# Performance work log

Measured on AMD Instinct MI355X. Metric: run time of the kernel, lower is better.

## Reference

```python
import jax, jax.numpy as jnp
import numpy as np

EPS_BN = 1e-5
NEG_SLOPE = 0.2

def _bn(x, gamma, beta):
    # BatchNorm1d using batch statistics (training-mode math, biased var as torch)
    mu = jnp.mean(x, axis=0)
    var = jnp.var(x, axis=0)
    return (x - mu) * jax.lax.rsqrt(var + EPS_BN) * gamma + beta

def _gat(x, src, dst, W, att_src, att_dst, bias, N):
    # x: [N, Fin]; W: [Fin, H*C]; att_*: [H, C]
    H, C = att_src.shape
    h = (x @ W).reshape(N, H, C)                       # [N,H,C]
    a_src = jnp.sum(h * att_src, axis=-1)              # [N,H]
    a_dst = jnp.sum(h * att_dst, axis=-1)              # [N,H]
    alpha = jax.nn.leaky_relu(a_src[src] + a_dst[dst], NEG_SLOPE)  # [E,H]
    # segment softmax over destination nodes
    m = jax.ops.segment_max(alpha, dst, num_segments=N)           # [N,H]
    e = jnp.exp(alpha - m[dst])
    s = jax.ops.segment_sum(e, dst, num_segments=N)
    a = e / (s[dst] + 1e-16)                           # [E,H]
    msg = h[src] * a[:, :, None]                       # [E,H,C]
    out = jax.ops.segment_sum(msg, dst, num_segments=N)  # [N,H,C]
    return out.reshape(N, H * C) + bias

def setup_inputs() -> dict:
    key = jax.random.key(0)
    ks = jax.random.split(key, 16)
    N, Fin, Hid = 50000, 128, 64
    E = 800000
    x = jax.random.normal(ks[0], (N, Fin), dtype=jnp.float32)
    edge_index = jax.random.randint(ks[1], (2, E), 0, N, dtype=jnp.int32)
    sc = 0.1
    return {
        'x': x,
        'edge_index': edge_index,
        'W1': jax.random.normal(ks[2], (Fin, 2 * Hid), jnp.float32) * sc,
        'att_src1': jax.random.normal(ks[3], (2, Hid), jnp.float32) * sc,
        'att_dst1': jax.random.normal(ks[4], (2, Hid), jnp.float32) * sc,
        'b1': jnp.zeros((2 * Hid,), jnp.float32),
        'g1': jnp.ones((2 * Hid,), jnp.float32),
        'be1': jnp.zeros((2 * Hid,), jnp.float32),
        'W2': jax.random.normal(ks[5], (2 * Hid, Hid), jnp.float32) * sc,
        'att_src2': jax.random.normal(ks[6], (1, Hid), jnp.float32) * sc,
        'att_dst2': jax.random.normal(ks[7], (1, Hid), jnp.float32) * sc,
        'b2': jnp.zeros((Hid,), jnp.float32),
        'g2': jnp.ones((Hid,), jnp.float32),
        'be2': jnp.zeros((Hid,), jnp.float32),
        'linW': jax.random.normal(ks[8], (Hid, 1), jnp.float32) * sc,
        'linb': jnp.zeros((1,), jnp.float32),
    }

def reference(x, edge_index, W1, att_src1, att_dst1, b1, g1, be1,
              W2, att_src2, att_dst2, b2, g2, be2, linW, linb):
    N = x.shape[0]
    loops = jnp.arange(N, dtype=edge_index.dtype)
    src = jnp.concatenate([edge_index[0], loops])  # PyG adds self-loops
    dst = jnp.concatenate([edge_index[1], loops])
    h = _gat(x, src, dst, W1, att_src1, att_dst1, b1, N)
    h = jax.nn.relu(_bn(h, g1, be1))                 # dropout = identity (eval)
    h = _gat(h, src, dst, W2, att_src2, att_dst2, b2, N)
    h = jax.nn.relu(_bn(h, g2, be2))
    return (h @ linW + linb).squeeze(-1)
```

## Files before the change

kernel.cpp:

```cpp
#include <hip/hip_runtime.h>
#include <hip/hip_fp16.h>
#include <math.h>

#define LEAKY 0.2f
#define XPAD 136
#define MAXB 512

typedef _Float16 f16x8 __attribute__((ext_vector_type(8)));
typedef float f32x4 __attribute__((ext_vector_type(4)));

__device__ inline int h2i(__half2 h) { union { __half2 h; int i; } u; u.h = h; return u.i; }
__device__ inline __half2 i2h(int i) { union { __half2 h; int i; } u; u.i = i; return u.h; }


__global__ __launch_bounds__(256) void k_bhist(const int* __restrict__ ei,
                                               int* __restrict__ gbcnt, int E, int PB)
{
  __shared__ int lh[MAXB];
  int t = threadIdx.x;
  for (int i = t; i < PB; i += 256) lh[i] = 0;
  __syncthreads();
  int base = blockIdx.x * 2048;
#pragma unroll
  for (int k = 0; k < 8; ++k) {
    int idx = base + t + k * 256;
    if (idx < E) atomicAdd(&lh[ei[E + idx] >> 7], 1);
  }
  __syncthreads();
  for (int i = t; i < PB; i += 256) if (lh[i]) atomicAdd(&gbcnt[i], lh[i]);
}

__global__ __launch_bounds__(512) void k_bscan(const int* __restrict__ gbcnt,
                                               int* __restrict__ pbase,
                                               int* __restrict__ gcur, int PB)
{
  __shared__ int ls[512];
  int t = threadIdx.x;
  int v = (t < PB) ? gbcnt[t] : 0;
  ls[t] = v;
  __syncthreads();
  for (int off = 1; off < 512; off <<= 1) {
    int u = (t >= off) ? ls[t - off] : 0;
    __syncthreads();
    ls[t] += u;
    __syncthreads();
  }
  int excl = ls[t] - v;
  if (t <= PB) pbase[t] = excl;
  if (t < PB) gcur[t] = excl;
}

__global__ __launch_bounds__(256) void k_part(const int* __restrict__ ei,
                                              int* __restrict__ gcur,
                                              int2* __restrict__ pairs, int E, int PB)
{
  __shared__ int lcnt[MAXB], lbase[MAXB];
  int t = threadIdx.x;
  for (int i = t; i < PB; i += 256) lcnt[i] = 0;
  __syncthreads();
  int base = blockIdx.x * 4096;
  int lp[16];
#pragma unroll
  for (int k = 0; k < 16; ++k) {
    int idx = base + t + k * 256;
    int pk = -1;
    if (idx < E) {
      int b = ei[E + idx] >> 7;
      int p = atomicAdd(&lcnt[b], 1);
      pk = (p << 10) | b;
    }
    lp[k] = pk;
  }
  __syncthreads();
  for (int b = t; b < PB; b += 256) lbase[b] = atomicAdd(&gcur[b], lcnt[b]);
  __syncthreads();
#pragma unroll
  for (int k = 0; k < 16; ++k) {
    if (lp[k] >= 0) {
      int idx = base + t + k * 256;
      int b = lp[k] & 1023, p = lp[k] >> 10;
      pairs[lbase[b] + p] = make_int2(ei[idx], ei[E + idx]);
    }
  }
}

__global__ __launch_bounds__(256) void k_fine(const int2* __restrict__ pairs,
                                              const int* __restrict__ pbase,
                                              int* __restrict__ rowptr,
                                              int* __restrict__ colx, int N)
{
  __shared__ int ldeg[128], lcur[128];
  int b = blockIdx.x, t = threadIdx.x;
  int nbase = b << 7;
  int nbn = N - nbase; if (nbn > 128) nbn = 128;
  if (t < 128) ldeg[t] = (t < nbn) ? 1 : 0;
  __syncthreads();
  int e0 = pbase[b], e1 = pbase[b + 1];
  for (int e = e0 + t; e < e1; e += 256) atomicAdd(&ldeg[pairs[e].y - nbase], 1);
  __syncthreads();
  int myv = (t < 128) ? ldeg[t] : 0;
  for (int off = 1; off < 128; off <<= 1) {
    int u = (t < 128 && t >= off) ? ldeg[t - off] : 0;
    __syncthreads();
    if (t < 128) ldeg[t] += u;
    __syncthreads();
  }
  int colx0 = e0 + nbase;
  if (t < 128) {
    int excl = ldeg[t] - myv;
    lcur[t] = colx0 + excl;
    int idx = nbase + t;
    if (idx <= N) rowptr[idx] = colx0 + excl;
  }
  __syncthreads();
  for (int e = e0 + t; e < e1; e += 256) {
    int2 p = pairs[e];
    int pos = atomicAdd(&lcur[p.y - nbase], 1);
    colx[pos] = p.x;
  }
  if (t < nbn) {
    int pos = atomicAdd(&lcur[t], 1);
    colx[pos] = nbase + t;
  }
}

__global__ __launch_bounds__(256) void k_gemm1(
    const float* __restrict__ x, const float* __restrict__ W,
    const float* __restrict__ att_s, const float* __restrict__ att_d,
    unsigned* __restrict__ h1h, float* __restrict__ a1s, float* __restrict__ a1d, int N)
{
  __shared__ __align__(16) _Float16 Xh[64 * XPAD];
  __shared__ __align__(16) _Float16 Wt[128 * XPAD];
  int t = threadIdx.x;
  const float4* W4 = (const float4*)W;
#pragma unroll
  for (int i = 0; i < 16; ++i) {
    int id = t + i * 256;
    int row = id >> 5, c0 = (id & 31) * 4;
    float4 wv = W4[id];
    Wt[(c0    ) * XPAD + row] = (_Float16)wv.x;
    Wt[(c0 + 1) * XPAD + row] = (_Float16)wv.y;
    Wt[(c0 + 2) * XPAD + row] = (_Float16)wv.z;
    Wt[(c0 + 3) * XPAD + row] = (_Float16)wv.w;
  }
  int row0 = blockIdx.x * 64;
  const float4* X4 = (const float4*)x;
#pragma unroll
  for (int i = 0; i < 8; ++i) {
    int id = t + i * 256;
    int r = id >> 5, c = id & 31;
    int gr = row0 + r;
    float4 v = (gr < N) ? X4[(size_t)gr * 32 + c] : make_float4(0.f, 0.f, 0.f, 0.f);
    unsigned p01 = (unsigned)h2i(__floats2half2_rn(v.x, v.y));
    unsigned p23 = (unsigned)h2i(__floats2half2_rn(v.z, v.w));
    *(uint2*)&Xh[r * XPAD + c * 4] = make_uint2(p01, p23);
  }
  __syncthreads();
  int w = t >> 6, l = t & 63;
  int m = l & 15, kg = l >> 4;
  f32x4 acc[8];
#pragma unroll
  for (int c = 0; c < 8; ++c) { acc[c][0] = 0.f; acc[c][1] = 0.f; acc[c][2] = 0.f; acc[c][3] = 0.f; }
#pragma unroll
  for (int ks = 0; ks < 4; ++ks) {
    f16x8 a = *(const f16x8*)&Xh[(w * 16 + m) * XPAD + ks * 32 + kg * 8];
#pragma unroll
    for (int c = 0; c < 8; ++c) {
      f16x8 bfr = *(const f16x8*)&Wt[(c * 16 + m) * XPAD + ks * 32 + kg * 8];
      acc[c] = __builtin_amdgcn_mfma_f32_16x16x32_f16(a, bfr, acc[c], 0, 0, 0);
    }
  }
#pragma unroll
  for (int c = 0; c < 8; ++c)
#pragma unroll
    for (int r = 0; r < 4; ++r)
      Xh[(w * 16 + kg * 4 + r) * XPAD + c * 16 + m] = (_Float16)acc[c][r];
  __syncthreads();
#pragma unroll
  for (int i = 0; i < 8; ++i) {
    int id = t + i * 256;
    int r = id >> 5, c4 = id & 31;
    int gr = row0 + r;
    uint2 pk = *(const uint2*)&Xh[r * XPAD + c4 * 4];
    float2 v01 = __half22float2(i2h((int)pk.x));
    float2 v23 = __half22float2(i2h((int)pk.y));
    int col = c4 * 4;
    float4 asv = *(const float4*)&att_s[col];
    float4 adv = *(const float4*)&att_d[col];
    float ps = v01.x * asv.x + v01.y * asv.y + v23.x * asv.z + v23.y * asv.w;
    float pd = v01.x * adv.x + v01.y * adv.y + v23.x * adv.z + v23.y * adv.w;
    ps += __shfl_xor(ps, 1); ps += __shfl_xor(ps, 2); ps += __shfl_xor(ps, 4); ps += __shfl_xor(ps, 8);
    pd += __shfl_xor(pd, 1); pd += __shfl_xor(pd, 2); pd += __shfl_xor(pd, 4); pd += __shfl_xor(pd, 8);
    if (gr < N) {
      *(uint2*)&h1h[(size_t)gr * 64 + c4 * 2] = pk;
      if ((t & 15) == 0) { int h = (t >> 4) & 1; a1s[gr * 2 + h] = ps; a1d[gr * 2 + h] = pd; }
    }
  }
}

__global__ __launch_bounds__(256) void k_agg1(
    const int* __restrict__ rowptr, const int* __restrict__ colx,
    const unsigned* __restrict__ h1h, const float* __restrict__ a1s,
    const float* __restrict__ a1d, const float* __restrict__ b1,
    unsigned* __restrict__ v1h, float* __restrict__ stats, int N)
{
  int t = threadIdx.x;
  int w = t >> 6, lane = t & 63;
  int g = lane >> 5, q = lane & 31;
  bool hi = q >= 16;
  int n = blockIdx.x * 8 + w * 2 + g;
  bool act = n < N;
  float4 bias = *(const float4*)&b1[q * 4];
  int start = 0, end = 0;
  float2 ad = make_float2(0.f, 0.f);
  if (act) { start = rowptr[n]; end = rowptr[n + 1]; ad = *(const float2*)&a1d[n * 2]; }
  float se = 0.f;
  float4 acc = {0, 0, 0, 0};
  for (int base = start; base < end; base += 32) {
    int cnt = end - base; if (cnt > 32) cnt = 32;
    int sl = 0, epk = 0;
    if (q < cnt) {
      sl = colx[base + q];
      float2 av = *(const float2*)&a1s[sl * 2];
      float x0 = av.x + ad.x, x1 = av.y + ad.y;
      x0 = (x0 > 0.f) ? x0 : LEAKY * x0;
      x1 = (x1 > 0.f) ? x1 : LEAKY * x1;
      epk = h2i(__floats2half2_rn(__expf(x0), __expf(x1)));
    }
    int j = 0;
    int lim16 = cnt & ~15;
    for (; j < lim16; j += 16) {
      int ss[16], ee[16];
#pragma unroll
      for (int k = 0; k < 16; ++k) { ss[k] = __shfl(sl, j + k, 32); ee[k] = __shfl(epk, j + k, 32); }
      uint2 rr[16];
#pragma unroll
      for (int k = 0; k < 16; ++k) rr[k] = *(const uint2*)&h1h[(size_t)ss[k] * 64 + q * 2];
#pragma unroll
      for (int k = 0; k < 16; ++k) {
        float2 ef = __half22float2(i2h(ee[k]));
        float wg = hi ? ef.y : ef.x;
        float2 r01 = __half22float2(i2h((int)rr[k].x));
        float2 r23 = __half22float2(i2h((int)rr[k].y));
        se += wg;
        acc.x = fmaf(wg, r01.x, acc.x);
        acc.y = fmaf(wg, r01.y, acc.y);
        acc.z = fmaf(wg, r23.x, acc.z);
        acc.w = fmaf(wg, r23.y, acc.w);
      }
    }
    int lim8 = cnt & ~7;
    for (; j < lim8; j += 8) {
      int ss[8], ee[8];
#pragma unroll
      for (int k = 0; k < 8; ++k) { ss[k] = __shfl(sl, j + k, 32); ee[k] = __shfl(epk, j + k, 32); }
      uint2 rr[8];
#pragma unroll
      for (int k = 0; k < 8; ++k) rr[k] = *(const uint2*)&h1h[(size_t)ss[k] * 64 + q * 2];
#pragma unroll
      for (int k = 0; k < 8; ++k) {
        float2 ef = __half22float2(i2h(ee[k]));
        float wg = hi ? ef.y : ef.x;
        float2 r01 = __half22float2(i2h((int)rr[k].x));
        float2 r23 = __half22float2(i2h((int)rr[k].y));
        se += wg;
        acc.x = fmaf(wg, r01.x, acc.x);
        acc.y = fmaf(wg, r01.y, acc.y);
        acc.z = fmaf(wg, r23.x, acc.z);
        acc.w = fmaf(wg, r23.y, acc.w);
      }
    }
    for (; j < cnt; ++j) {
      int s0 = __shfl(sl, j, 32), e0 = __shfl(epk, j, 32);
      float2 ef = __half22float2(i2h(e0));
      float wg = hi ? ef.y : ef.x;
      uint2 rv = *(const uint2*)&h1h[(size_t)s0 * 64 + q * 2];
      float2 r01 = __half22float2(i2h((int)rv.x));
      float2 r23 = __half22float2(i2h((int)rv.y));
      se += wg;
      acc.x = fmaf(wg, r01.x, acc.x);
      acc.y = fmaf(wg, r01.y, acc.y);
      acc.z = fmaf(wg, r23.x, acc.z);
      acc.w = fmaf(wg, r23.y, acc.w);
    }
  }
  float4 o = {0, 0, 0, 0};
  if (act) {
    float inv = 1.f / se;
    o.x = fmaf(acc.x, inv, bias.x);
    o.y = fmaf(acc.y, inv, bias.y);
    o.z = fmaf(acc.z, inv, bias.z);
    o.w = fmaf(acc.w, inv, bias.w);
    unsigned p01 = (unsigned)h2i(__floats2half2_rn(o.x, o.y));
    unsigned p23 = (unsigned)h2i(__floats2half2_rn(o.z, o.w));
    *(uint2*)&v1h[(size_t)n * 64 + q * 2] = make_uint2(p01, p23);
  }
  __shared__ float4 reds[4][64], redq[4][64];
  reds[w][lane] = o;
  redq[w][lane] = make_float4(o.x * o.x, o.y * o.y, o.z * o.z, o.w * o.w);
  __syncthreads();
  if (t < 128) {
    int qq = t >> 2, ii = t & 3;
    float s = 0.f, sq = 0.f;
#pragma unroll
    for (int w2 = 0; w2 < 4; ++w2) {
      s  += (&reds[w2][qq].x)[ii] + (&reds[w2][qq + 32].x)[ii];
      sq += (&redq[w2][qq].x)[ii] + (&redq[w2][qq + 32].x)[ii];
    }
    int sl8 = (blockIdx.x & 7) * 256;
    atomicAdd(&stats[sl8 + t], s);
    atomicAdd(&stats[sl8 + 128 + t], sq);
  }
}

__global__ __launch_bounds__(256) void k_gemm2(
    const unsigned* __restrict__ v1h, const float* __restrict__ W2,
    const float* __restrict__ stats, const float* __restrict__ g1, const float* __restrict__ be1,
    const float* __restrict__ att_s, const float* __restrict__ att_d,
    unsigned* __restrict__ h2h, float* __restrict__ a2s, float* __restrict__ a2d,
    int N, float rcpN)
{
  __shared__ __align__(16) _Float16 Xh[64 * XPAD];
  __shared__ __align__(16) _Float16 Wt[64 * XPAD];
  __shared__ float kc[128], sc[128];
  int t = threadIdx.x;
  if (t < 128) {
    float su = 0.f, sq = 0.f;
#pragma unroll
    for (int s8 = 0; s8 < 8; ++s8) { su += stats[s8 * 256 + t]; sq += stats[s8 * 256 + 128 + t]; }
    float mu = su * rcpN;
    float var = sq * rcpN - mu * mu;
    float kk = g1[t] * rsqrtf(var + 1e-5f);
    kc[t] = kk; sc[t] = be1[t] - mu * kk;
  }
  const float4* W4 = (const float4*)W2;
#pragma unroll
  for (int i = 0; i < 8; ++i) {
    int id = t + i * 256;
    int row = id >> 4, c0 = (id & 15) * 4;
    float4 wv = W4[id];
    Wt[(c0    ) * XPAD + row] = (_Float16)wv.x;
    Wt[(c0 + 1) * XPAD + row] = (_Float16)wv.y;
    Wt[(c0 + 2) * XPAD + row] = (_Float16)wv.z;
    Wt[(c0 + 3) * XPAD + row] = (_Float16)wv.w;
  }
  __syncthreads();
  int row0 = blockIdx.x * 64;
#pragma unroll
  for (int i = 0; i < 8; ++i) {
    int id = t + i * 256;
    int r = id >> 5, c4 = id & 31;
    int gr = row0 + r;
    uint2 pv = (gr < N) ? *(const uint2*)&v1h[(size_t)gr * 64 + c4 * 2] : make_uint2(0, 0);
    float2 a01 = __half22float2(i2h((int)pv.x));
    float2 a23 = __half22float2(i2h((int)pv.y));
    int f0 = c4 * 4;
    float o0 = fmaxf(a01.x * kc[f0]     + sc[f0],     0.f);
    float o1 = fmaxf(a01.y * kc[f0 + 1] + sc[f0 + 1], 0.f);
    float o2 = fmaxf(a23.x * kc[f0 + 2] + sc[f0 + 2], 0.f);
    float o3 = fmaxf(a23.y * kc[f0 + 3] + sc[f0 + 3], 0.f);
    unsigned p01 = (unsigned)h2i(__floats2half2_rn(o0, o1));
    unsigned p23 = (unsigned)h2i(__floats2half2_rn(o2, o3));
    *(uint2*)&Xh[r * XPAD + c4 * 4] = make_uint2(p01, p23);
  }
  __syncthreads();
  int w = t >> 6, l = t & 63;
  int m = l & 15, kg = l >> 4;
  f32x4 acc[4];
#pragma unroll
  for (int c = 0; c < 4; ++c) { acc[c][0] = 0.f; acc[c][1] = 0.f; acc[c][2] = 0.f; acc[c][3] = 0.f; }
#pragma unroll
  for (int ks = 0; ks < 4; ++ks) {
    f16x8 a = *(const f16x8*)&Xh[(w * 16 + m) * XPAD + ks * 32 + kg * 8];
#pragma unroll
    for (int c = 0; c < 4; ++c) {
      f16x8 bfr = *(const f16x8*)&Wt[(c * 16 + m) * XPAD + ks * 32 + kg * 8];
      acc[c] = __builtin_amdgcn_mfma_f32_16x16x32_f16(a, bfr, acc[c], 0, 0, 0);
    }
  }
#pragma unroll
  for (int c = 0; c < 4; ++c)
#pragma unroll
    for (int r = 0; r < 4; ++r)
      Xh[(w * 16 + kg * 4 + r) * XPAD + c * 16 + m] = (_Float16)acc[c][r];
  __syncthreads();
#pragma unroll
  for (int i = 0; i < 4; ++i) {
    int id = t + i * 256;
    int r = id >> 4, c4 = id & 15;
    int gr = row0 + r;
    uint2 pk = *(const uint2*)&Xh[r * XPAD + c4 * 4];
    float2 v01 = __half22float2(i2h((int)pk.x));
    float2 v23 = __half22float2(i2h((int)pk.y));
    int col = c4 * 4;
    float4 asv = *(const float4*)&att_s[col];
    float4 adv = *(const float4*)&att_d[col];
    float ps = v01.x * asv.x + v01.y * asv.y + v23.x * asv.z + v23.y * asv.w;
    float pd = v01.x * adv.x + v01.y * adv.y + v23.x * adv.z + v23.y * adv.w;
    ps += __shfl_xor(ps, 1); ps += __shfl_xor(ps, 2); ps += __shfl_xor(ps, 4); ps += __shfl_xor(ps, 8);
    pd += __shfl_xor(pd, 1); pd += __shfl_xor(pd, 2); pd += __shfl_xor(pd, 4); pd += __shfl_xor(pd, 8);
    if (gr < N) {
      *(uint2*)&h2h[(size_t)gr * 32 + c4 * 2] = pk;
      if ((t & 15) == 0) { a2s[gr] = ps; a2d[gr] = pd; }
    }
  }
}

__global__ __launch_bounds__(256) void k_agg2(
    const int* __restrict__ rowptr, const int* __restrict__ colx,
    const unsigned* __restrict__ h2h, const float* __restrict__ a2s,
    const float* __restrict__ a2d, const float* __restrict__ b2,
    unsigned* __restrict__ v2h, float* __restrict__ stats, int N)
{
  int t = threadIdx.x;
  int w = t >> 6, lane = t & 63;
  int g = lane >> 4, q = lane & 15;
  int n = blockIdx.x * 16 + w * 4 + g;
  bool act = n < N;
  float4 bias = *(const float4*)&b2[q * 4];
  int start = 0, end = 0;
  float ad = 0.f;
  if (act) { start = rowptr[n]; end = rowptr[n + 1]; ad = a2d[n]; }
  float se = 0.f;
  float4 acc = {0, 0, 0, 0};
  for (int base = start; base < end; base += 16) {
    int cnt = end - base; if (cnt > 16) cnt = 16;
    int sl = 0; float ev = 0.f;
    if (q < cnt) {
      sl = colx[base + q];
      float av = a2s[sl] + ad;
      av = (av > 0.f) ? av : LEAKY * av;
      ev = __expf(av);
    }
    int j = 0;
    if (cnt == 16) {
      int ss[16]; float ee[16];
#pragma unroll
      for (int k = 0; k < 16; ++k) { ss[k] = __shfl(sl, k, 16); ee[k] = __shfl(ev, k, 16); }
      uint2 rr[16];
#pragma unroll
      for (int k = 0; k < 16; ++k) rr[k] = *(const uint2*)&h2h[(size_t)ss[k] * 32 + q * 2];
#pragma unroll
      for (int k = 0; k < 16; ++k) {
        float2 r01 = __half22float2(i2h((int)rr[k].x));
        float2 r23 = __half22float2(i2h((int)rr[k].y));
        se += ee[k];
        acc.x = fmaf(ee[k], r01.x, acc.x);
        acc.y = fmaf(ee[k], r01.y, acc.y);
        acc.z = fmaf(ee[k], r23.x, acc.z);
        acc.w = fmaf(ee[k], r23.y, acc.w);
      }
      j = 16;
    }
    int lim8 = cnt & ~7;
    for (; j < lim8; j += 8) {
      int ss[8]; float ee[8];
#pragma unroll
      for (int k = 0; k < 8; ++k) { ss[k] = __shfl(sl, j + k, 16); ee[k] = __shfl(ev, j + k, 16); }
      uint2 rr[8];
#pragma unroll
      for (int k = 0; k < 8; ++k) rr[k] = *(const uint2*)&h2h[(size_t)ss[k] * 32 + q * 2];
#pragma unroll
      for (int k = 0; k < 8; ++k) {
        float2 r01 = __half22float2(i2h((int)rr[k].x));
        float2 r23 = __half22float2(i2h((int)rr[k].y));
        se += ee[k];
        acc.x = fmaf(ee[k], r01.x, acc.x);
        acc.y = fmaf(ee[k], r01.y, acc.y);
        acc.z = fmaf(ee[k], r23.x, acc.z);
        acc.w = fmaf(ee[k], r23.y, acc.w);
      }
    }
    for (; j < cnt; ++j) {
      int s0 = __shfl(sl, j, 16);
      float e0 = __shfl(ev, j, 16);
      uint2 rv = *(const uint2*)&h2h[(size_t)s0 * 32 + q * 2];
      float2 r01 = __half22float2(i2h((int)rv.x));
      float2 r23 = __half22float2(i2h((int)rv.y));
      se += e0;
      acc.x = fmaf(e0, r01.x, acc.x);
      acc.y = fmaf(e0, r01.y, acc.y);
      acc.z = fmaf(e0, r23.x, acc.z);
      acc.w = fmaf(e0, r23.y, acc.w);
    }
  }
  float4 o = {0, 0, 0, 0};
  if (act) {
    float inv = 1.f / se;
    o.x = fmaf(acc.x, inv, bias.x);
    o.y = fmaf(acc.y, inv, bias.y);
    o.z = fmaf(acc.z, inv, bias.z);
    o.w = fmaf(acc.w, inv, bias.w);
    unsigned p01 = (unsigned)h2i(__floats2half2_rn(o.x, o.y));
    unsigned p23 = (unsigned)h2i(__floats2half2_rn(o.z, o.w));
    *(uint2*)&v2h[(size_t)n * 32 + q * 2] = make_uint2(p01, p23);
  }
  __shared__ float4 reds[4][64], redq[4][64];
  reds[w][lane] = o;
  redq[w][lane] = make_float4(o.x * o.x, o.y * o.y, o.z * o.z, o.w * o.w);
  __syncthreads();
  if (t < 64) {
    int qq = t >> 2, ii = t & 3;
    float s = 0.f, sq = 0.f;
#pragma unroll
    for (int w2 = 0; w2 < 4; ++w2) {
#pragma unroll
      for (int g2 = 0; g2 < 4; ++g2) {
        s  += (&reds[w2][g2 * 16 + qq].x)[ii];
        sq += (&redq[w2][g2 * 16 + qq].x)[ii];
      }
    }
    int sl8 = (blockIdx.x & 7) * 128;
    atomicAdd(&stats[sl8 + t], s);
    atomicAdd(&stats[sl8 + 64 + t], sq);
  }
}

__global__ __launch_bounds__(256) void k_out(
    const unsigned* __restrict__ v2h, const float* __restrict__ stats,
    const float* __restrict__ g2, const float* __restrict__ be2,
    const float* __restrict__ linW, const float* __restrict__ linb,
    float* __restrict__ out, int N, float rcpN)
{
  __shared__ float kc[64], sc[64], lw[64];
  int t = threadIdx.x;
  if (t < 64) {
    float su = 0.f, sq = 0.f;
#pragma unroll
    for (int s8 = 0; s8 < 8; ++s8) { su += stats[s8 * 128 + t]; sq += stats[s8 * 128 + 64 + t]; }
    float mu = su * rcpN;
    float var = sq * rcpN - mu * mu;
    float kk = g2[t] * rsqrtf(var + 1e-5f);
    kc[t] = kk; sc[t] = be2[t] - mu * kk; lw[t] = linW[t];
  }
  __syncthreads();
  int w = t >> 6, lane = t & 63, g = lane >> 5, q = lane & 31;
  int n = blockIdx.x * 8 + w * 2 + g;
  if (n >= N) return;
  unsigned uv = v2h[(size_t)n * 32 + q];
  float2 vf = __half22float2(i2h((int)uv));
  float h0 = fmaxf(vf.x * kc[2 * q] + sc[2 * q], 0.f);
  float h1 = fmaxf(vf.y * kc[2 * q + 1] + sc[2 * q + 1], 0.f);
  float p = fmaf(h0, lw[2 * q], h1 * lw[2 * q + 1]);
#pragma unroll
  for (int off = 16; off; off >>= 1) p += __shfl_xor(p, off, 32);
  if (q == 0) out[n] = p + linb[0];
}

extern "C" void kernel_launch(void* const* d_in, const int* in_sizes, int n_in,
                              void* d_out, int out_size, void* d_ws, size_t ws_size,
                              hipStream_t stream)
{
  const float* x    = (const float*)d_in[0];
  const int*   ei   = (const int*)d_in[1];
  const float* W1   = (const float*)d_in[2];
  const float* as1  = (const float*)d_in[3];
  const float* ad1  = (const float*)d_in[4];
  const float* b1   = (const float*)d_in[5];
  const float* g1   = (const float*)d_in[6];
  const float* be1  = (const float*)d_in[7];
  const float* W2   = (const float*)d_in[8];
  const float* as2  = (const float*)d_in[9];
  const float* ad2  = (const float*)d_in[10];
  const float* b2   = (const float*)d_in[11];
  const float* g2   = (const float*)d_in[12];
  const float* be2  = (const float*)d_in[13];
  const float* linW = (const float*)d_in[14];
  const float* linb = (const float*)d_in[15];
  float* out = (float*)d_out;

  int N = in_sizes[0] / 128;
  int E = in_sizes[1] / 2;
  int Etot = E + N;
  float rcpN = 1.f / (float)N;
  int PB = (N + 127) / 128;

  float* ws = (float*)d_ws;
  size_t o = 0;
  float* H1HF = ws + o; o += (size_t)N * 64;
  float* V1HF = ws + o; o += (size_t)N * 64;
  float* A1S  = ws + o; o += (size_t)N * 2;
  float* A1D  = ws + o; o += (size_t)N * 2;
  float* A2S  = ws + o; o += N;
  float* A2D  = ws + o; o += N;
  float* ST1  = ws + o; o += 8 * 256;
  float* ST2  = ws + o; o += 8 * 128;
  int* GBCNT  = (int*)(ws + o); o += MAXB;
  int* PBASE  = (int*)(ws + o); o += MAXB + 1;
  int* GCUR   = (int*)(ws + o); o += MAXB;
  int* ROWPTR = (int*)(ws + o); o += (size_t)N + 1;
  int* COL    = (int*)(ws + o); o += (size_t)Etot;
  int2* PAIRS = (int2*)(ws + o); o += (size_t)E * 2;
  unsigned* H1H = (unsigned*)H1HF;
  unsigned* H2H = (unsigned*)H1HF;
  unsigned* V1H = (unsigned*)V1HF;
  unsigned* V2H = (unsigned*)V1HF;

  hipMemsetAsync(ST1, 0, (3072 + MAXB) * 4, stream);

  int gb  = (N + 63) / 64;
  int bh  = (E + 2047) / 2048;
  int pt  = (E + 4095) / 4096;
  int ab1 = (N + 7) / 8;
  int ab2 = (N + 15) / 16;
  int ob  = (N + 7) / 8;

  k_bhist<<<bh, 256, 0, stream>>>(ei, GBCNT, E, PB);
  k_bscan<<<1, 512, 0, stream>>>(GBCNT, PBASE, GCUR, PB);
  k_part<<<pt, 256, 0, stream>>>(ei, GCUR, PAIRS, E, PB);
  k_fine<<<PB, 256, 0, stream>>>(PAIRS, PBASE, ROWPTR, COL, N);
  k_gemm1<<<gb, 256, 0, stream>>>(x, W1, as1, ad1, H1H, A1S, A1D, N);
  k_agg1<<<ab1, 256, 0, stream>>>(ROWPTR, COL, H1H, A1S, A1D, b1, V1H, ST1, N);
  k_gemm2<<<gb, 256, 0, stream>>>(V1H, W2, ST1, g1, be1, as2, ad2, H2H, A2S, A2D, N, rcpN);
  k_agg2<<<ab2, 256, 0, stream>>>(ROWPTR, COL, H2H, A2S, A2D, b2, V2H, ST2, N);
  k_out<<<ob, 256, 0, stream>>>(V2H, ST2, g2, be2, linW, linb, out, N, rcpN);
}
```

Baseline: 170.8 us.

## Widen agg1 gathers to 16-byte loads and split BatchNorm stats into separate kernels

The layer-1 aggregation kernel now assigns 16 lanes per destination node instead of 32. Each lane gathers a 16-byte chunk of the fp16 source row, which doubles the nodes per block and halves the shuffle and index overhead per edge. The BatchNorm sum and sum-of-squares reductions are moved out of both aggregation kernels into a templated k_stats kernel that rereads the fp16 outputs, which simplifies the aggregation epilogue but adds two launches and an extra pass over the activations. The statistics are now computed from fp16-rounded values rather than fp32 ones. k_part also keeps the src and dst indices in registers instead of reloading them from global memory for the scatter.

Result: slower. 179.5 us (+5.1%).

```diff
diff --git a/kernel.cpp b/kernel.cpp
--- a/kernel.cpp
+++ b/kernel.cpp
@@ -11,7 +11,6 @@
 
 __device__ inline int h2i(__half2 h) { union { __half2 h; int i; } u; u.h = h; return u.i; }
 __device__ inline __half2 i2h(int i) { union { __half2 h; int i; } u; u.i = i; return u.h; }
-
 
 __global__ __launch_bounds__(256) void k_bhist(const int* __restrict__ ei,
                                                int* __restrict__ gbcnt, int E, int PB)
@@ -59,17 +58,18 @@
   for (int i = t; i < PB; i += 256) lcnt[i] = 0;
   __syncthreads();
   int base = blockIdx.x * 4096;
-  int lp[16];
+  int lsrc[16], ldst[16], lp[16];
 #pragma unroll
   for (int k = 0; k < 16; ++k) {
     int idx = base + t + k * 256;
-    int pk = -1;
+    lp[k] = -1;
     if (idx < E) {
-      int b = ei[E + idx] >> 7;
+      int s = ei[idx], d = ei[E + idx];
+      lsrc[k] = s; ldst[k] = d;
+      int b = d >> 7;
       int p = atomicAdd(&lcnt[b], 1);
-      pk = (p << 10) | b;
-    }
-    lp[k] = pk;
+      lp[k] = (p << 10) | b;
+    }
   }
   __syncthreads();
   for (int b = t; b < PB; b += 256) lbase[b] = atomicAdd(&gcur[b], lcnt[b]);
@@ -77,9 +77,8 @@
 #pragma unroll
   for (int k = 0; k < 16; ++k) {
     if (lp[k] >= 0) {
-      int idx = base + t + k * 256;
       int b = lp[k] & 1023, p = lp[k] >> 10;
-      pairs[lbase[b] + p] = make_int2(ei[idx], ei[E + idx]);
+      pairs[lbase[b] + p] = make_int2(lsrc[k], ldst[k]);
     }
   }
 }
@@ -202,22 +201,23 @@
     const int* __restrict__ rowptr, const int* __restrict__ colx,
     const unsigned* __restrict__ h1h, const float* __restrict__ a1s,
     const float* __restrict__ a1d, const float* __restrict__ b1,
-    unsigned* __restrict__ v1h, float* __restrict__ stats, int N)
+    unsigned* __restrict__ v1h, int N)
 {
   int t = threadIdx.x;
   int w = t >> 6, lane = t & 63;
-  int g = lane >> 5, q = lane & 31;
-  bool hi = q >= 16;
-  int n = blockIdx.x * 8 + w * 2 + g;
+  int g = lane >> 4, q = lane & 15;
+  bool hi = q >= 8;
+  int n = blockIdx.x * 16 + w * 4 + g;
   bool act = n < N;
-  float4 bias = *(const float4*)&b1[q * 4];
+  float4 biasA = *(const float4*)&b1[q * 8];
+  float4 biasB = *(const float4*)&b1[q * 8 + 4];
   int start = 0, end = 0;
   float2 ad = make_float2(0.f, 0.f);
   if (act) { start = rowptr[n]; end = rowptr[n + 1]; ad = *(const float2*)&a1d[n * 2]; }
   float se = 0.f;
-  float4 acc = {0, 0, 0, 0};
-  for (int base = start; base < end; base += 32) {
-    int cnt = end - base; if (cnt > 32) cnt = 32;
+  float4 accA = {0, 0, 0, 0}, accB = {0, 0, 0, 0};
+  for (int base = start; base < end; base += 16) {
+    int cnt = end - base; if (cnt > 16) cnt = 16;
     int sl = 0, epk = 0;
     if (q < cnt) {
       sl = colx[base + q];
@@ -228,88 +228,115 @@
       epk = h2i(__floats2half2_rn(__expf(x0), __expf(x1)));
     }
     int j = 0;
-    int lim16 = cnt & ~15;
-    for (; j < lim16; j += 16) {
+    if (cnt == 16) {
       int ss[16], ee[16];
 #pragma unroll
-      for (int k = 0; k < 16; ++k) { ss[k] = __shfl(sl, j + k, 32); ee[k] = __shfl(epk, j + k, 32); }
-      uint2 rr[16];
-#pragma unroll
-      for (int k = 0; k < 16; ++k) rr[k] = *(const uint2*)&h1h[(size_t)ss[k] * 64 + q * 2];
+      for (int k = 0; k < 16; ++k) { ss[k] = __shfl(sl, k, 16); ee[k] = __shfl(epk, k, 16); }
+      uint4 rr[16];
+#pragma unroll
+      for (int k = 0; k < 16; ++k) rr[k] = *(const uint4*)&h1h[(size_t)ss[k] * 64 + q * 4];
 #pragma unroll
       for (int k = 0; k < 16; ++k) {
         float2 ef = __half22float2(i2h(ee[k]));
         float wg = hi ? ef.y : ef.x;
-        float2 r01 = __half22float2(i2h((int)rr[k].x));
-        float2 r23 = __half22float2(i2h((int)rr[k].y));
+        float2 r0 = __half22float2(i2h((int)rr[k].x));
+        float2 r1 = __half22float2(i2h((int)rr[k].y));
+        float2 r2 = __half22float2(i2h((int)rr[k].z));
+        float2 r3 = __half22float2(i2h((int)rr[k].w));
         se += wg;
-        acc.x = fmaf(wg, r01.x, acc.x);
-        acc.y = fmaf(wg, r01.y, acc.y);
-        acc.z = fmaf(wg, r23.x, acc.z);
-        acc.w = fmaf(wg, r23.y, acc.w);
+        accA.x = fmaf(wg, r0.x, accA.x); accA.y = fmaf(wg, r0.y, accA.y);
+        accA.z = fmaf(wg, r1.x, accA.z); accA.w = fmaf(wg, r1.y, accA.w);
+        accB.x = fmaf(wg, r2.x, accB.x); accB.y = fmaf(wg, r2.y, accB.y);
+        accB.z = fmaf(wg, r3.x, accB.z); accB.w = fmaf(wg, r3.y, accB.w);
       }
+      j = 16;
     }
     int lim8 = cnt & ~7;
     for (; j < lim8; j += 8) {
       int ss[8], ee[8];
 #pragma unroll
-      for (int k = 0; k < 8; ++k) { ss[k] = __shfl(sl, j + k, 32); ee[k] = __shfl(epk, j + k, 32); }
-      uint2 rr[8];
-#pragma unroll
-      for (int k = 0; k < 8; ++k) rr[k] = *(const uint2*)&h1h[(size_t)ss[k] * 64 + q * 2];
+      for (int k = 0; k < 8; ++k) { ss[k] = __shfl(sl, j + k, 16); ee[k] = __shfl(epk, j + k, 16); }
+      uint4 rr[8];
+#pragma unroll
+      for (int k = 0; k < 8; ++k) rr[k] = *(const uint4*)&h1h[(size_t)ss[k] * 64 + q * 4];
 #pragma unroll
       for (int k = 0; k < 8; ++k) {
         float2 ef = __half22float2(i2h(ee[k]));
         float wg = hi ? ef.y : ef.x;
-        float2 r01 = __half22float2(i2h((int)rr[k].x));
-        float2 r23 = __half22float2(i2h((int)rr[k].y));
+        float2 r0 = __half22float2(i2h((int)rr[k].x));
+        float2 r1 = __half22float2(i2h((int)rr[k].y));
+        float2 r2 = __half22float2(i2h((int)rr[k].z));
+        float2 r3 = __half22float2(i2h((int)rr[k].w));
         se += wg;
-        acc.x = fmaf(wg, r01.x, acc.x);
-        acc.y = fmaf(wg, r01.y, acc.y);
-        acc.z = fmaf(wg, r23.x, acc.z);
-        acc.w = fmaf(wg, r23.y, acc.w);
+        accA.x = fmaf(wg, r0.x, accA.x); accA.y = fmaf(wg, r0.y, accA.y);
+        accA.z = fmaf(wg, r1.x, accA.z); accA.w = fmaf(wg, r1.y, accA.w);
+        accB.x = fmaf(wg, r2.x, accB.x); accB.y = fmaf(wg, r2.y, accB.y);
+        accB.z = fmaf(wg, r3.x, accB.z); accB.w = fmaf(wg, r3.y, accB.w);
       }
     }
     for (; j < cnt; ++j) {
-      int s0 = __shfl(sl, j, 32), e0 = __shfl(epk, j, 32);
+      int s0 = __shfl(sl, j, 16), e0 = __shfl(epk, j, 16);
       float2 ef = __half22float2(i2h(e0));
       float wg = hi ? ef.y : ef.x;
-      uint2 rv = *(const uint2*)&h1h[(size_t)s0 * 64 + q * 2];
-      float2 r01 = __half22float2(i2h((int)rv.x));
-      float2 r23 = __half22float2(i2h((int)rv.y));
+      uint4 rv = *(const uint4*)&h1h[(size_t)s0 * 64 + q * 4];
+      float2 r0 = __half22float2(i2h((int)rv.x));
+      float2 r1 = __half22float2(i2h((int)rv.y));
+      float2 r2 = __half22float2(i2h((int)rv.z));
+      float2 r3 = __half22float2(i2h((int)rv.w));
       se += wg;
-      acc.x = fmaf(wg, r01.x, acc.x);
-      acc.y = fmaf(wg, r01.y, acc.y);
-      acc.z = fmaf(wg, r23.x, acc.z);
-      acc.w = fmaf(wg, r23.y, acc.w);
-    }
-  }
-  float4 o = {0, 0, 0, 0};
+      accA.x = fmaf(wg, r0.x, accA.x); accA.y = fmaf(wg, r0.y, accA.y);
+      accA.z = fmaf(wg, r1.x, accA.z); accA.w = fmaf(wg, r1.y, accA.w);
+      accB.x = fmaf(wg, r2.x, accB.x); accB.y = fmaf(wg, r2.y, accB.y);
+      accB.z = fmaf(wg, r3.x, accB.z); accB.w = fmaf(wg, r3.y, accB.w);
+    }
+  }
   if (act) {
     float inv = 1.f / se;
-    o.x = fmaf(acc.x, inv, bias.x);
-    o.y = fmaf(acc.y, inv, bias.y);
-    o.z = fmaf(acc.z, inv, bias.z);
-    o.w = fmaf(acc.w, inv, bias.w);
-    unsigned p01 = (unsigned)h2i(__floats2half2_rn(o.x, o.y));
-    unsigned p23 = (unsigned)h2i(__floats2half2_rn(o.z, o.w));
-    *(uint2*)&v1h[(size_t)n * 64 + q * 2] = make_uint2(p01, p23);
-  }
-  __shared__ float4 reds[4][64], redq[4][64];
-  reds[w][lane] = o;
-  redq[w][lane] = make_float4(o.x * o.x, o.y * o.y, o.z * o.z, o.w * o.w);
-  __syncthreads();
-  if (t < 128) {
-    int qq = t >> 2, ii = t & 3;
-    float s = 0.f, sq = 0.f;
-#pragma unroll
-    for (int w2 = 0; w2 < 4; ++w2) {
-      s  += (&reds[w2][qq].x)[ii] + (&reds[w2][qq + 32].x)[ii];
-      sq += (&redq[w2][qq].x)[ii] + (&redq[w2][qq + 32].x)[ii];
-    }
-    int sl8 = (blockIdx.x & 7) * 256;
-    atomicAdd(&stats[sl8 + t], s);
-    atomicAdd(&stats[sl8 + 128 + t], sq);
+    float4 oA, oB;
+    oA.x = fmaf(accA.x, inv, biasA.x);
+    oA.y = fmaf(accA.y, inv, biasA.y);
+    oA.z = fmaf(accA.z, inv, biasA.z);
+    oA.w = fmaf(accA.w, inv, biasA.w);
+    oB.x = fmaf(accB.x, inv, biasB.x);
+    oB.y = fmaf(accB.y, inv, biasB.y);
+    oB.z = fmaf(accB.z, inv, biasB.z);
+    oB.w = fmaf(accB.w, inv, biasB.w);
+    unsigned p0 = (unsigned)h2i(__floats2half2_rn(oA.x, oA.y));
+    unsigned p1 = (unsigned)h2i(__floats2half2_rn(oA.z, oA.w));
+    unsigned p2 = (unsigned)h2i(__floats2half2_rn(oB.x, oB.y));
+    unsigned p3 = (unsigned)h2i(__floats2half2_rn(oB.z, oB.w));
+    *(uint4*)&v1h[(size_t)n * 64 + q * 4] = make_uint4(p0, p1, p2, p3);
+  }
+}
+
+template<int UPR>
+__global__ __launch_bounds__(256) void k_stats(const unsigned* __restrict__ vh,
+                                               float* __restrict__ stats, int N)
+{
+  const int F = UPR * 2, RPB = 256 / UPR;
+  int t = threadIdx.x;
+  int q = t & (UPR - 1), rg = t / UPR;
+  float s0 = 0.f, s1 = 0.f, q0 = 0.f, q1 = 0.f;
+  for (int n = blockIdx.x * RPB + rg; n < N; n += 256 * RPB) {
+    float2 vf = __half22float2(i2h((int)vh[(size_t)n * UPR + q]));
+    s0 += vf.x; q0 += vf.x * vf.x;
+    s1 += vf.y; q1 += vf.y * vf.y;
+  }
+  __shared__ float4 red[256];
+  red[t] = make_float4(s0, s1, q0, q1);
+  __syncthreads();
+  if (t < UPR) {
+    float4 a = red[t];
+#pragma unroll
+    for (int g2 = 1; g2 < RPB; ++g2) {
+      float4 b = red[t + g2 * UPR];
+      a.x += b.x; a.y += b.y; a.z += b.z; a.w += b.w;
+    }
+    int sl = (blockIdx.x & 7) * 2 * F;
+    atomicAdd(&stats[sl + 2 * t], a.x);
+    atomicAdd(&stats[sl + 2 * t + 1], a.y);
+    atomicAdd(&stats[sl + F + 2 * t], a.z);
+    atomicAdd(&stats[sl + F + 2 * t + 1], a.w);
   }
 }
 
@@ -410,7 +437,7 @@
     const int* __restrict__ rowptr, const int* __restrict__ colx,
     const unsigned* __restrict__ h2h, const float* __restrict__ a2s,
     const float* __restrict__ a2d, const float* __restrict__ b2,
-    unsigned* __restrict__ v2h, float* __restrict__ stats, int N)
+    unsigned* __restrict__ v2h, int N)
 {
   int t = threadIdx.x;
   int w = t >> 6, lane = t & 63;
@@ -484,9 +511,9 @@
       acc.w = fmaf(e0, r23.y, acc.w);
     }
   }
-  float4 o = {0, 0, 0, 0};
   if (act) {
     float inv = 1.f / se;
+    float4 o;
     o.x = fmaf(acc.x, inv, bias.x);
     o.y = fmaf(acc.y, inv, bias.y);
     o.z = fmaf(acc.z, inv, bias.z);
@@ -494,25 +521,6 @@
     unsigned p01 = (unsigned)h2i(__floats2half2_rn(o.x, o.y));
     unsigned p23 = (unsigned)h2i(__floats2half2_rn(o.z, o.w));
     *(uint2*)&v2h[(size_t)n * 32 + q * 2] = make_uint2(p01, p23);
-  }
-  __shared__ float4 reds[4][64], redq[4][64];
-  reds[w][lane] = o;
-  redq[w][lane] = make_float4(o.x * o.x, o.y * o.y, o.z * o.z, o.w * o.w);
-  __syncthreads();
-  if (t < 64) {
-    int qq = t >> 2, ii = t & 3;
-    float s = 0.f, sq = 0.f;
-#pragma unroll
-    for (int w2 = 0; w2 < 4; ++w2) {
-#pragma unroll
-      for (int g2 = 0; g2 < 4; ++g2) {
-        s  += (&reds[w2][g2 * 16 + qq].x)[ii];
-        sq += (&redq[w2][g2 * 16 + qq].x)[ii];
-      }
-    }
-    int sl8 = (blockIdx.x & 7) * 128;
-    atomicAdd(&stats[sl8 + t], s);
-    atomicAdd(&stats[sl8 + 64 + t], sq);
   }
 }
 
@@ -601,7 +609,7 @@
   int gb  = (N + 63) / 64;
   int bh  = (E + 2047) / 2048;
   int pt  = (E + 4095) / 4096;
-  int ab1 = (N + 7) / 8;
+  int ab1 = (N + 15) / 16;
   int ab2 = (N + 15) / 16;
   int ob  = (N + 7) / 8;
 
@@ -610,8 +618,10 @@
   k_part<<<pt, 256, 0, stream>>>(ei, GCUR, PAIRS, E, PB);
   k_fine<<<PB, 256, 0, stream>>>(PAIRS, PBASE, ROWPTR, COL, N);
   k_gemm1<<<gb, 256, 0, stream>>>(x, W1, as1, ad1, H1H, A1S, A1D, N);
-  k_agg1<<<ab1, 256, 0, stream>>>(ROWPTR, COL, H1H, A1S, A1D, b1, V1H, ST1, N);
+  k_agg1<<<ab1, 256, 0, stream>>>(ROWPTR, COL, H1H, A1S, A1D, b1, V1H, N);
+  k_stats<64><<<256, 256, 0, stream>>>(V1H, ST1, N);
   k_gemm2<<<gb, 256, 0, stream>>>(V1H, W2, ST1, g1, be1, as2, ad2, H2H, A2S, A2D, N, rcpN);
-  k_agg2<<<ab2, 256, 0, stream>>>(ROWPTR, COL, H2H, A2S, A2D, b2, V2H, ST2, N);
+  k_agg2<<<ab2, 256, 0, stream>>>(ROWPTR, COL, H2H, A2S, A2D, b2, V2H, N);
+  k_stats<32><<<256, 256, 0, stream>>>(V2H, ST2, N);
   k_out<<<ob, 256, 0, stream>>>(V2H, ST2, g2, be2, linW, linb, out, N, rcpN);
 }
```
